# Performance work log

Hardware: AMD Instinct MI355X
Metric: run time of the kernel (lower is better)

## Reference

```python
import jax, jax.numpy as jnp
import numpy as np

N_WIRES = 10
N_BLOCKS = 4
DIM = 2 ** N_WIRES


def _tables(n):
    # Basis-state bit tables. Wire 0 is the most-significant bit (torchquantum convention).
    s = np.arange(2 ** n)
    bits = (s[None, :] >> (n - 1 - np.arange(n))[:, None]) & 1  # [n, 2^n]
    zval = (1 - 2 * bits).astype(np.float32)  # PauliZ eigenvalue per wire per basis state
    # Composition of the circular CNOT ring (0,1),(1,2),...,(n-2,n-1),(n-1,0)
    # as a single basis permutation: state'[s] = state[P[s]].
    pairs = [(i, i + 1) for i in range(n - 1)] + [(n - 1, 0)]
    P = s.copy()
    for c, t in pairs:
        bit = (s >> (n - 1 - c)) & 1
        g = s ^ (bit << (n - 1 - t))  # CNOT maps new[s] = old[g(s)]
        P = P[g]
    return zval, P


_ZVAL_NP, _PERM_NP = _tables(N_WIRES)


def setup_inputs() -> dict:
    key = jax.random.key(0)
    k1, k2 = jax.random.split(key)
    x = jax.random.normal(k1, (2048, N_WIRES), jnp.float32)
    params = jax.random.normal(k2, (N_BLOCKS, 6, N_WIRES), jnp.float32)
    return {"x": x, "params": params}


def _rz_all(state, theta, zval):
    # RZ(theta_w) on every wire fused into one diagonal phase over the full statevector.
    # RZ = diag(e^{-i t/2}, e^{+i t/2}); exponent sign = -zval (bit0 -> -1).
    phase = jnp.exp((-0.5j) * (theta @ zval).astype(jnp.complex64))  # [2^n]
    return state * phase[None, :]


def _ry_all(state, theta, bsz):
    # RY(theta_w) on each wire w: 2x2 rotation applied along that wire's axis.
    for w in range(N_WIRES):
        left = 2 ** w
        right = DIM // (2 * left)
        s4 = state.reshape(bsz, left, 2, right)
        c = jnp.cos(theta[w] * 0.5)
        s_ = jnp.sin(theta[w] * 0.5)
        U = jnp.stack([jnp.stack([c, -s_]), jnp.stack([s_, c])]).astype(jnp.complex64)
        s4 = jnp.einsum('bixk,jx->bijk', s4, U)
        state = s4.reshape(bsz, DIM)
    return state


def reference(x, params):
    zval = jnp.asarray(_ZVAL_NP)
    perm = jnp.asarray(_PERM_NP)
    bsz = x.shape[0]
    state = jnp.zeros((bsz, DIM), jnp.complex64).at[:, 0].set(1.0)  # |0...0>
    for k in range(N_BLOCKS):
        p = params[k]
        # NOTE: the original module's "rx" layers are constructed with tq.RZ,
        # so each block is RZ, RY, RZ, CNOT-ring, RZ, RY, RZ, CNOT-ring.
        state = _rz_all(state, p[0], zval)
        state = _ry_all(state, p[1], bsz)
        state = _rz_all(state, p[2], zval)
        state = state[:, perm]
        state = _rz_all(state, p[3], zval)
        state = _ry_all(state, p[4], bsz)
        state = _rz_all(state, p[5], zval)
        state = state[:, perm]
        if k != N_BLOCKS - 1:
            # data re-uploading encoder: RZ(x[:, w]) on wire w, batch-dependent diagonal
            enc = jnp.exp((-0.5j) * (x @ zval).astype(jnp.complex64))  # [B, 2^n]
            state = state * enc
    probs = state.real ** 2 + state.imag ** 2  # [B, 2^n]
    out = probs @ zval.T  # MeasureAll PauliZ -> [B, n_wires]
    return out[None]  # [1, B, n_wires]
```

## Files before the change

kernel.cpp:

```cpp
#include <hip/hip_runtime.h>

#define NW 10

template<int CTRL>
__device__ __forceinline__ float dpp_qperm(float v) {
    return __int_as_float(__builtin_amdgcn_mov_dpp(__float_as_int(v), CTRL, 0xF, 0xF, true));
}

__global__ __launch_bounds__(128) void qsim_kernel(const float* __restrict__ x,
                                                   const float* __restrict__ params,
                                                   float* __restrict__ out) {
    __shared__ float bre[1024];
    __shared__ float bim[1024];
    __shared__ float sred[2][NW];

    const int t     = threadIdx.x;
    const int W     = t >> 6;
    const int lane  = t & 63;
    const int b     = blockIdx.x;
    const int sbase = (W << 9) | (lane << 3);
    const int abase = lane | (W << 9);

    float re[8], im[8];
#pragma unroll
    for (int r = 0; r < 8; ++r) { re[r] = 0.f; im[r] = 0.f; }
    if (t == 0) re[0] = 1.f;

    const float* xb = x + b * NW;

    auto diag = [&](const float th[NW]) {
        float A = 0.f;
#pragma unroll
        for (int w = 0; w < NW; ++w) A += th[w];
        float hi = -0.5f * A + (W ? th[0] : 0.f);
#pragma unroll
        for (int j = 0; j < 6; ++j)
            hi += ((lane >> j) & 1) ? th[6 - j] : 0.f;
        float lo[8];
        lo[0] = 0.f;           lo[1] = th[9];
        lo[2] = th[8];         lo[3] = th[8] + th[9];
        lo[4] = th[7];         lo[5] = th[7] + th[9];
        lo[6] = th[7] + th[8]; lo[7] = th[7] + th[8] + th[9];
#pragma unroll
        for (int r = 0; r < 8; ++r) {
            float sn, cs;
            __sincosf(hi + lo[r], &sn, &cs);
            float a = re[r], bb = im[r];
            re[r] = a * cs - bb * sn;
            im[r] = a * sn + bb * cs;
        }
    };

    auto ry = [&](const float* __restrict__ th) {
#pragma unroll
        for (int kb = 0; kb < 3; ++kb) {
            float sn, cs;
            __sincosf(0.5f * th[9 - kb], &sn, &cs);
            const int m = 1 << kb;
#pragma unroll
            for (int r = 0; r < 8; ++r) {
                if (!(r & m)) {
                    const int r2 = r | m;
                    float a = re[r], bb = re[r2];
                    re[r]  = cs * a - sn * bb;
                    re[r2] = sn * a + cs * bb;
                    float ai = im[r], bi = im[r2];
                    im[r]  = cs * ai - sn * bi;
                    im[r2] = sn * ai + cs * bi;
                }
            }
        }
        {
            float sn, cs; __sincosf(0.5f * th[6], &sn, &cs);
            const float ss = (lane & 1) ? sn : -sn;
#pragma unroll
            for (int r = 0; r < 8; ++r) {
                float pre = dpp_qperm<0xB1>(re[r]);
                float pim = dpp_qperm<0xB1>(im[r]);
                re[r] = cs * re[r] + ss * pre;
                im[r] = cs * im[r] + ss * pim;
            }
        }
        {
            float sn, cs; __sincosf(0.5f * th[5], &sn, &cs);
            const float ss = (lane & 2) ? sn : -sn;
#pragma unroll
            for (int r = 0; r < 8; ++r) {
                float pre = dpp_qperm<0x4E>(re[r]);
                float pim = dpp_qperm<0x4E>(im[r]);
                re[r] = cs * re[r] + ss * pre;
                im[r] = cs * im[r] + ss * pim;
            }
        }
#pragma unroll
        for (int j = 2; j < 6; ++j) {
            float sn, cs; __sincosf(0.5f * th[6 - j], &sn, &cs);
            const float ss = ((lane >> j) & 1) ? sn : -sn;
#pragma unroll
            for (int r = 0; r < 8; ++r) {
                float pre = __shfl_xor(re[r], 1 << j, 64);
                float pim = __shfl_xor(im[r], 1 << j, 64);
                re[r] = cs * re[r] + ss * pre;
                im[r] = cs * im[r] + ss * pim;
            }
        }
        {
            float sn, cs; __sincosf(0.5f * th[0], &sn, &cs);
            const float ss = W ? sn : -sn;
#pragma unroll
            for (int r = 0; r < 8; ++r) {
                bre[abase + (r << 6)] = re[r];
                bim[abase + (r << 6)] = im[r];
            }
            __syncthreads();
            const int pb = abase ^ 512;
#pragma unroll
            for (int r = 0; r < 8; ++r) {
                float pre = bre[pb + (r << 6)];
                float pim = bim[pb + (r << 6)];
                re[r] = cs * re[r] + ss * pre;
                im[r] = cs * im[r] + ss * pim;
            }
            __syncthreads();
        }
    };

    auto perm = [&]() {
#pragma unroll
        for (int r = 0; r < 8; ++r) {
            bre[abase + (r << 6)] = re[r];
            bim[abase + (r << 6)] = im[r];
        }
        __syncthreads();
#pragma unroll
        for (int r = 0; r < 8; ++r) {
            const int s = sbase + r;
            const int q = s ^ (s >> 1) ^ ((r & 1) * 0x300);
            const int a = ((q >> 3) & 63) | ((q & 7) << 6) | ((q >> 9) << 9);
            re[r] = bre[a];
            im[r] = bim[a];
        }
        __syncthreads();
    };

#pragma unroll 1
    for (int k = 0; k < 4; ++k) {
        const float* p = params + k * 6 * NW;
        float th[NW];
        if (k > 0) {
#pragma unroll
            for (int w = 0; w < NW; ++w) th[w] = p[w] + xb[w];
            diag(th);
        }
        ry(p + NW);
#pragma unroll
        for (int w = 0; w < NW; ++w) th[w] = p[2 * NW + w];
        diag(th);
        perm();
#pragma unroll
        for (int w = 0; w < NW; ++w) th[w] = p[3 * NW + w];
        diag(th);
        ry(p + 4 * NW);
        if (k < 3) {
#pragma unroll
            for (int w = 0; w < NW; ++w) th[w] = p[5 * NW + w];
            diag(th);
        }
        perm();
    }

    float pr[8];
#pragma unroll
    for (int r = 0; r < 8; ++r) pr[r] = re[r] * re[r] + im[r] * im[r];
    float S = 0.f;
#pragma unroll
    for (int r = 0; r < 8; ++r) S += pr[r];

    float acc[NW];
    acc[0] = W ? -S : S;
#pragma unroll
    for (int w = 1; w <= 6; ++w) {
        const int j = 6 - w;
        acc[w] = ((lane >> j) & 1) ? -S : S;
    }
#pragma unroll
    for (int w = 7; w < NW; ++w) {
        const int kb = 9 - w;
        float tt = 0.f;
#pragma unroll
        for (int r = 0; r < 8; ++r)
            tt += ((r >> kb) & 1) ? -pr[r] : pr[r];
        acc[w] = tt;
    }
#pragma unroll
    for (int w = 0; w < NW; ++w) {
        float a = acc[w];
        a += dpp_qperm<0xB1>(a);
        a += dpp_qperm<0x4E>(a);
        a += __shfl_xor(a, 4, 64);
        a += __shfl_xor(a, 8, 64);
        a += __shfl_xor(a, 16, 64);
        a += __shfl_xor(a, 32, 64);
        acc[w] = a;
    }
    if (lane == 0) {
#pragma unroll
        for (int w = 0; w < NW; ++w) sred[W][w] = acc[w];
    }
    __syncthreads();
    if (t < NW) out[b * NW + t] = sred[0][t] + sred[1][t];
}

extern "C" void kernel_launch(void* const* d_in, const int* in_sizes, int n_in,
                              void* d_out, int out_size, void* d_ws, size_t ws_size,
                              hipStream_t stream) {
    const float* x      = (const float*)d_in[0];
    const float* params = (const float*)d_in[1];
    float* out          = (float*)d_out;
    (void)in_sizes; (void)n_in; (void)out_size; (void)d_ws; (void)ws_size;
    qsim_kernel<<<2048, 128, 0, stream>>>(x, params, out);
}
```

Measured before the change: 97.04 us.

## Precompute parameter phase tables in a prepass kernel and double-buffer shared exchange

Adds a precompute kernel that builds per-basis-state cos/sin tables for every parameter-only RZ diagonal and the RY cos/sin pairs, so the main kernel loads them from global memory (likely L2-resident) instead of calling sincos per amplitude. The x-dependent encoder phase is computed once per batch row and combined with the table. Shared-memory exchanges are double-buffered to drop the trailing barrier, lane shuffles use DPP and ds_swizzle instead of generic shuffles, and float2 interleaved storage is used. The trade is extra global loads, a second launch, and a workspace dependency.

```diff
diff --git a/kernel.cpp b/kernel.cpp
--- a/kernel.cpp
+++ b/kernel.cpp
@@ -3,169 +3,242 @@
 #define NW 10
 
 template<int CTRL>
-__device__ __forceinline__ float dpp_qperm(float v) {
+__device__ __forceinline__ float fdpp(float v) {
     return __int_as_float(__builtin_amdgcn_mov_dpp(__float_as_int(v), CTRL, 0xF, 0xF, true));
 }
-
-__global__ __launch_bounds__(128) void qsim_kernel(const float* __restrict__ x,
-                                                   const float* __restrict__ params,
-                                                   float* __restrict__ out) {
-    __shared__ float bre[1024];
-    __shared__ float bim[1024];
+template<int PAT>
+__device__ __forceinline__ float fswz(float v) {
+    return __int_as_float(__builtin_amdgcn_ds_swizzle(__float_as_int(v), PAT));
+}
+
+__global__ void precompute_kernel(const float* __restrict__ params, float2* __restrict__ tab) {
+    const int d = blockIdx.x;
+    const int j = threadIdx.x;
+    if (d < 14) {
+        int k, row;
+        if (d < 3)       { k = d + 1;  row = 0; }
+        else if (d < 7)  { k = d - 3;  row = 2; }
+        else if (d < 11) { k = d - 7;  row = 3; }
+        else             { k = d - 11; row = 5; }
+        const float* th = params + (k * 6 + row) * NW;
+        const int s = (((j >> 6) & 1) << 9) | ((j & 63) << 3) | (j >> 7);
+        float ang = 0.f;
+#pragma unroll
+        for (int w = 0; w < NW; ++w)
+            ang += th[w] * (((s >> (9 - w)) & 1) ? 0.5f : -0.5f);
+        float sn, cs;
+        __sincosf(ang, &sn, &cs);
+        tab[d * 1024 + j] = make_float2(cs, sn);
+    } else if (j < 80) {
+        const int ry = j / NW, w = j % NW;
+        const int k = ry >> 1, i = ry & 1;
+        const float* th = params + (k * 6 + (i ? 4 : 1)) * NW;
+        float sn, cs;
+        __sincosf(0.5f * th[w], &sn, &cs);
+        tab[14 * 1024 + j] = make_float2(cs, sn);
+    }
+}
+
+__global__ __launch_bounds__(128, 4) void qsim_kernel(const float* __restrict__ x,
+                                                      const float2* __restrict__ tab,
+                                                      float* __restrict__ out) {
+    __shared__ float2 buf[2][1024];
     __shared__ float sred[2][NW];
 
     const int t     = threadIdx.x;
     const int W     = t >> 6;
     const int lane  = t & 63;
     const int b     = blockIdx.x;
-    const int sbase = (W << 9) | (lane << 3);
-    const int abase = lane | (W << 9);
+    const int ebase = lane | (W << 6);
+    const float2* ry_tab = tab + 14 * 1024;
 
     float re[8], im[8];
 #pragma unroll
     for (int r = 0; r < 8; ++r) { re[r] = 0.f; im[r] = 0.f; }
     if (t == 0) re[0] = 1.f;
 
+    int geidx[8];
+#pragma unroll
+    for (int r = 0; r < 8; ++r) {
+        const int s = (W << 9) | (lane << 3) | r;
+        const int q = s ^ (s >> 1) ^ ((r & 1) * 0x300);
+        geidx[r] = ((q >> 3) & 63) | (((q >> 9) & 1) << 6) | ((q & 7) << 7);
+    }
+
     const float* xb = x + b * NW;
-
-    auto diag = [&](const float th[NW]) {
+    float xr[8], xi[8];
+    {
+        float xv[NW];
+#pragma unroll
+        for (int w = 0; w < NW; ++w) xv[w] = xb[w];
         float A = 0.f;
 #pragma unroll
-        for (int w = 0; w < NW; ++w) A += th[w];
-        float hi = -0.5f * A + (W ? th[0] : 0.f);
+        for (int w = 0; w < NW; ++w) A += xv[w];
+        float hi = -0.5f * A + (W ? xv[0] : 0.f);
 #pragma unroll
         for (int j = 0; j < 6; ++j)
-            hi += ((lane >> j) & 1) ? th[6 - j] : 0.f;
+            hi += ((lane >> j) & 1) ? xv[6 - j] : 0.f;
         float lo[8];
-        lo[0] = 0.f;           lo[1] = th[9];
-        lo[2] = th[8];         lo[3] = th[8] + th[9];
-        lo[4] = th[7];         lo[5] = th[7] + th[9];
-        lo[6] = th[7] + th[8]; lo[7] = th[7] + th[8] + th[9];
+        lo[0] = 0.f;             lo[1] = xv[9];
+        lo[2] = xv[8];           lo[3] = xv[8] + xv[9];
+        lo[4] = xv[7];           lo[5] = xv[7] + xv[9];
+        lo[6] = xv[7] + xv[8];   lo[7] = xv[7] + xv[8] + xv[9];
+#pragma unroll
+        for (int r = 0; r < 8; ++r)
+            __sincosf(hi + lo[r], &xi[r], &xr[r]);
+    }
+
+    int bs = 0;
+
+    auto tdiag = [&](int d) {
+        const float2* tb = tab + (d << 10) + ebase;
 #pragma unroll
         for (int r = 0; r < 8; ++r) {
-            float sn, cs;
-            __sincosf(hi + lo[r], &sn, &cs);
-            float a = re[r], bb = im[r];
-            re[r] = a * cs - bb * sn;
-            im[r] = a * sn + bb * cs;
-        }
-    };
-
-    auto ry = [&](const float* __restrict__ th) {
+            const float2 p = tb[r << 7];
+            const float a = re[r], bb = im[r];
+            re[r] = a * p.x - bb * p.y;
+            im[r] = a * p.y + bb * p.x;
+        }
+    };
+    auto txdiag = [&](int d) {
+        const float2* tb = tab + (d << 10) + ebase;
+#pragma unroll
+        for (int r = 0; r < 8; ++r) {
+            const float2 p = tb[r << 7];
+            const float cx = p.x * xr[r] - p.y * xi[r];
+            const float sx = p.x * xi[r] + p.y * xr[r];
+            const float a = re[r], bb = im[r];
+            re[r] = a * cx - bb * sx;
+            im[r] = a * sx + bb * cx;
+        }
+    };
+
+    auto ry = [&](int ridx) {
+        const float2* rt = ry_tab + ridx * NW;
 #pragma unroll
         for (int kb = 0; kb < 3; ++kb) {
-            float sn, cs;
-            __sincosf(0.5f * th[9 - kb], &sn, &cs);
+            const float2 cw = rt[9 - kb];
             const int m = 1 << kb;
 #pragma unroll
             for (int r = 0; r < 8; ++r) {
                 if (!(r & m)) {
                     const int r2 = r | m;
                     float a = re[r], bb = re[r2];
-                    re[r]  = cs * a - sn * bb;
-                    re[r2] = sn * a + cs * bb;
+                    re[r]  = cw.x * a - cw.y * bb;
+                    re[r2] = cw.y * a + cw.x * bb;
                     float ai = im[r], bi = im[r2];
-                    im[r]  = cs * ai - sn * bi;
-                    im[r2] = sn * ai + cs * bi;
+                    im[r]  = cw.x * ai - cw.y * bi;
+                    im[r2] = cw.y * ai + cw.x * bi;
                 }
             }
         }
         {
-            float sn, cs; __sincosf(0.5f * th[6], &sn, &cs);
-            const float ss = (lane & 1) ? sn : -sn;
-#pragma unroll
-            for (int r = 0; r < 8; ++r) {
-                float pre = dpp_qperm<0xB1>(re[r]);
-                float pim = dpp_qperm<0xB1>(im[r]);
-                re[r] = cs * re[r] + ss * pre;
-                im[r] = cs * im[r] + ss * pim;
-            }
-        }
-        {
-            float sn, cs; __sincosf(0.5f * th[5], &sn, &cs);
-            const float ss = (lane & 2) ? sn : -sn;
-#pragma unroll
-            for (int r = 0; r < 8; ++r) {
-                float pre = dpp_qperm<0x4E>(re[r]);
-                float pim = dpp_qperm<0x4E>(im[r]);
-                re[r] = cs * re[r] + ss * pre;
-                im[r] = cs * im[r] + ss * pim;
-            }
-        }
-#pragma unroll
-        for (int j = 2; j < 6; ++j) {
-            float sn, cs; __sincosf(0.5f * th[6 - j], &sn, &cs);
-            const float ss = ((lane >> j) & 1) ? sn : -sn;
-#pragma unroll
-            for (int r = 0; r < 8; ++r) {
-                float pre = __shfl_xor(re[r], 1 << j, 64);
-                float pim = __shfl_xor(im[r], 1 << j, 64);
-                re[r] = cs * re[r] + ss * pre;
-                im[r] = cs * im[r] + ss * pim;
-            }
-        }
-        {
-            float sn, cs; __sincosf(0.5f * th[0], &sn, &cs);
-            const float ss = W ? sn : -sn;
-#pragma unroll
-            for (int r = 0; r < 8; ++r) {
-                bre[abase + (r << 6)] = re[r];
-                bim[abase + (r << 6)] = im[r];
-            }
+            const float2 cw = rt[6];
+            const float ss = (lane & 1) ? cw.y : -cw.y;
+#pragma unroll
+            for (int r = 0; r < 8; ++r) {
+                float pre = fdpp<0xB1>(re[r]);
+                float pim = fdpp<0xB1>(im[r]);
+                re[r] = cw.x * re[r] + ss * pre;
+                im[r] = cw.x * im[r] + ss * pim;
+            }
+        }
+        {
+            const float2 cw = rt[5];
+            const float ss = (lane & 2) ? cw.y : -cw.y;
+#pragma unroll
+            for (int r = 0; r < 8; ++r) {
+                float pre = fdpp<0x4E>(re[r]);
+                float pim = fdpp<0x4E>(im[r]);
+                re[r] = cw.x * re[r] + ss * pre;
+                im[r] = cw.x * im[r] + ss * pim;
+            }
+        }
+        {
+            const float2 cw = rt[4];
+            const float ss = (lane & 4) ? cw.y : -cw.y;
+#pragma unroll
+            for (int r = 0; r < 8; ++r) {
+                float pre = fswz<0x101F>(re[r]);
+                float pim = fswz<0x101F>(im[r]);
+                re[r] = cw.x * re[r] + ss * pre;
+                im[r] = cw.x * im[r] + ss * pim;
+            }
+        }
+        {
+            const float2 cw = rt[3];
+            const float ss = (lane & 8) ? cw.y : -cw.y;
+#pragma unroll
+            for (int r = 0; r < 8; ++r) {
+                float pre = fdpp<0x128>(re[r]);
+                float pim = fdpp<0x128>(im[r]);
+                re[r] = cw.x * re[r] + ss * pre;
+                im[r] = cw.x * im[r] + ss * pim;
+            }
+        }
+        {
+            const float2 cw = rt[2];
+            const float ss = (lane & 16) ? cw.y : -cw.y;
+#pragma unroll
+            for (int r = 0; r < 8; ++r) {
+                float pre = fswz<0x401F>(re[r]);
+                float pim = fswz<0x401F>(im[r]);
+                re[r] = cw.x * re[r] + ss * pre;
+                im[r] = cw.x * im[r] + ss * pim;
+            }
+        }
+        {
+            const float2 cw = rt[1];
+            const float ss = (lane & 32) ? cw.y : -cw.y;
+#pragma unroll
+            for (int r = 0; r < 8; ++r) {
+                float pre = __shfl_xor(re[r], 32, 64);
+                float pim = __shfl_xor(im[r], 32, 64);
+                re[r] = cw.x * re[r] + ss * pre;
+                im[r] = cw.x * im[r] + ss * pim;
+            }
+        }
+        {
+            const float2 cw = rt[0];
+            float2* B = buf[bs]; bs ^= 1;
+#pragma unroll
+            for (int r = 0; r < 8; ++r)
+                B[ebase + (r << 7)] = make_float2(re[r], im[r]);
             __syncthreads();
-            const int pb = abase ^ 512;
-#pragma unroll
-            for (int r = 0; r < 8; ++r) {
-                float pre = bre[pb + (r << 6)];
-                float pim = bim[pb + (r << 6)];
-                re[r] = cs * re[r] + ss * pre;
-                im[r] = cs * im[r] + ss * pim;
-            }
-            __syncthreads();
+            const float ss = W ? cw.y : -cw.y;
+            const int pb = ebase ^ 64;
+#pragma unroll
+            for (int r = 0; r < 8; ++r) {
+                const float2 p = B[pb + (r << 7)];
+                re[r] = cw.x * re[r] + ss * p.x;
+                im[r] = cw.x * im[r] + ss * p.y;
+            }
         }
     };
 
     auto perm = [&]() {
+        float2* B = buf[bs]; bs ^= 1;
+#pragma unroll
+        for (int r = 0; r < 8; ++r)
+            B[ebase + (r << 7)] = make_float2(re[r], im[r]);
+        __syncthreads();
 #pragma unroll
         for (int r = 0; r < 8; ++r) {
-            bre[abase + (r << 6)] = re[r];
-            bim[abase + (r << 6)] = im[r];
-        }
-        __syncthreads();
-#pragma unroll
-        for (int r = 0; r < 8; ++r) {
-            const int s = sbase + r;
-            const int q = s ^ (s >> 1) ^ ((r & 1) * 0x300);
-            const int a = ((q >> 3) & 63) | ((q & 7) << 6) | ((q >> 9) << 9);
-            re[r] = bre[a];
-            im[r] = bim[a];
-        }
-        __syncthreads();
+            const float2 p = B[geidx[r]];
+            re[r] = p.x;
+            im[r] = p.y;
+        }
     };
 
 #pragma unroll 1
     for (int k = 0; k < 4; ++k) {
-        const float* p = params + k * 6 * NW;
-        float th[NW];
-        if (k > 0) {
-#pragma unroll
-            for (int w = 0; w < NW; ++w) th[w] = p[w] + xb[w];
-            diag(th);
-        }
-        ry(p + NW);
-#pragma unroll
-        for (int w = 0; w < NW; ++w) th[w] = p[2 * NW + w];
-        diag(th);
+        if (k > 0) txdiag(k - 1);
+        ry(2 * k);
+        tdiag(3 + k);
         perm();
-#pragma unroll
-        for (int w = 0; w < NW; ++w) th[w] = p[3 * NW + w];
-        diag(th);
-        ry(p + 4 * NW);
-        if (k < 3) {
-#pragma unroll
-            for (int w = 0; w < NW; ++w) th[w] = p[5 * NW + w];
-            diag(th);
-        }
+        tdiag(7 + k);
+        ry(2 * k + 1);
+        if (k < 3) tdiag(11 + k);
         perm();
     }
 
@@ -195,11 +268,11 @@
 #pragma unroll
     for (int w = 0; w < NW; ++w) {
         float a = acc[w];
-        a += dpp_qperm<0xB1>(a);
-        a += dpp_qperm<0x4E>(a);
-        a += __shfl_xor(a, 4, 64);
-        a += __shfl_xor(a, 8, 64);
-        a += __shfl_xor(a, 16, 64);
+        a += fdpp<0xB1>(a);
+        a += fdpp<0x4E>(a);
+        a += fswz<0x101F>(a);
+        a += fdpp<0x128>(a);
+        a += fswz<0x401F>(a);
         a += __shfl_xor(a, 32, 64);
         acc[w] = a;
     }
@@ -217,6 +290,8 @@
     const float* x      = (const float*)d_in[0];
     const float* params = (const float*)d_in[1];
     float* out          = (float*)d_out;
-    (void)in_sizes; (void)n_in; (void)out_size; (void)d_ws; (void)ws_size;
-    qsim_kernel<<<2048, 128, 0, stream>>>(x, params, out);
-}
+    float2* tab         = (float2*)d_ws;
+    (void)in_sizes; (void)n_in; (void)out_size; (void)ws_size;
+    precompute_kernel<<<15, 1024, 0, stream>>>(params, tab);
+    qsim_kernel<<<2048, 128, 0, stream>>>(x, tab, out);
+}
```

Result: faster. 86.31 us (-11.1%).
